# Optimization experiments

Measured on AMD Instinct MI355X. Metric: run time of the kernel, lower is better.

The kernel has to match this reference:

```python
import jax, jax.numpy as jnp
from jax import lax
import numpy as np

B, T, H, K = 128, 256, 768, 64


def setup_inputs() -> dict:
    key = jax.random.key(0)
    k1, k2, k3, k4 = jax.random.split(key, 4)
    hidden = jax.random.normal(k1, (B, T, H), dtype=jnp.float32)
    masks = jnp.ones((B, T), dtype=jnp.int32)
    target = jax.random.randint(k2, (B, T), 0, K, dtype=jnp.int32)
    W = jax.random.normal(k3, (H, K), dtype=jnp.float32) * 0.02
    b = jnp.zeros((K,), dtype=jnp.float32)
    transitions = jax.random.uniform(k4, (K, K), dtype=jnp.float32)
    return {"hidden": hidden, "masks": masks, "target": target,
            "W": W, "b": b, "transitions": transitions}


def _crf_log_norm(emissions, trans, seq_len):
    # emissions: [B,T,K]; forward algorithm (log-sum-exp recurrence over time)
    Tn = emissions.shape[1]
    alpha0 = emissions[:, 0]  # [B,K]

    def step(alpha, xs):
        emis_t, t = xs
        new = jax.nn.logsumexp(alpha[:, :, None] + trans[None], axis=1) + emis_t
        alpha = jnp.where((t < seq_len)[:, None], new, alpha)
        return alpha, None

    xs = (jnp.swapaxes(emissions[:, 1:], 0, 1), jnp.arange(1, Tn))
    alpha, _ = lax.scan(step, alpha0, xs)
    return jax.nn.logsumexp(alpha, axis=1)  # [B]


def _crf_sequence_score(emissions, tags, trans, seq_len):
    Tn = emissions.shape[1]
    t_idx = jnp.arange(Tn)
    valid = t_idx[None, :] < seq_len[:, None]  # [B,T]
    unary = jnp.take_along_axis(emissions, tags[..., None], axis=2)[..., 0]
    unary = jnp.sum(jnp.where(valid, unary, 0.0), axis=1)
    pair = trans[tags[:, :-1], tags[:, 1:]]  # [B,T-1]
    valid_pair = t_idx[1:][None, :] < seq_len[:, None]
    binary = jnp.sum(jnp.where(valid_pair, pair, 0.0), axis=1)
    return unary + binary


def _crf_decode(emissions, trans, seq_len):
    # Viterbi with backpointers; padded steps carry state (identity backptr)
    Bn, Tn, Kn = emissions.shape
    v0 = emissions[:, 0]

    def step(v, xs):
        emis_t, t = xs
        scores = v[:, :, None] + trans[None]  # [B, K_prev, K_cur]
        bp = jnp.argmax(scores, axis=1).astype(jnp.int32)
        new_v = jnp.max(scores, axis=1) + emis_t
        m = (t < seq_len)[:, None]
        v = jnp.where(m, new_v, v)
        bp = jnp.where(m, bp, jnp.arange(Kn, dtype=jnp.int32)[None])
        return v, bp

    xs = (jnp.swapaxes(emissions[:, 1:], 0, 1), jnp.arange(1, Tn))
    v, bps = lax.scan(step, v0, xs)  # bps: [T-1, B, K]
    best_score = jnp.max(v, axis=1)
    last_tag = jnp.argmax(v, axis=1).astype(jnp.int32)

    def back(tag, bp_t):
        prev = jnp.take_along_axis(bp_t, tag[:, None], axis=1)[:, 0]
        return prev, prev

    _, rev_tags = lax.scan(back, last_tag, bps, reverse=True)  # [T-1, B]
    path = jnp.concatenate([rev_tags, last_tag[None]], axis=0)  # [T, B]
    path = jnp.swapaxes(path, 0, 1)  # [B, T]
    valid = jnp.arange(Tn)[None, :] < seq_len[:, None]
    path = jnp.where(valid, path, 0)
    return path, best_score


def reference(hidden, masks, target, W, b, transitions):
    # dense projection (dropout omitted for determinism)
    emissions = jnp.einsum('bth,hk->btk', hidden, W) + b  # [B,T,K]
    seq_len = jnp.sum(masks, axis=1).astype(jnp.int32)
    log_norm = _crf_log_norm(emissions, transitions, seq_len)
    seq_score = _crf_sequence_score(emissions, target, transitions, seq_len)
    log_likelihood = seq_score - log_norm  # [B]
    decode_predict, _crf_scores = _crf_decode(emissions, transitions, seq_len)
    return decode_predict, log_likelihood
```

## Files before the change

kernel.cpp:

```cpp
#include <hip/hip_runtime.h>

#define B_ 128
#define T_ 256
#define H_ 768
#define K_ 64
#define BT_ (B_ * T_)

template <int CTRL>
__device__ __forceinline__ float dpp_mov_f(float x) {
    return __int_as_float(__builtin_amdgcn_update_dpp(
        __float_as_int(x), __float_as_int(x), CTRL, 0xF, 0xF, false));
}
__device__ __forceinline__ float wave_max64(float x) {
    x = fmaxf(x, dpp_mov_f<0x111>(x));
    x = fmaxf(x, dpp_mov_f<0x112>(x));
    x = fmaxf(x, dpp_mov_f<0x114>(x));
    x = fmaxf(x, dpp_mov_f<0x118>(x));
    x = fmaxf(x, dpp_mov_f<0x142>(x));
    x = fmaxf(x, dpp_mov_f<0x143>(x));
    return __int_as_float(__builtin_amdgcn_readlane(__float_as_int(x), 63));
}
__device__ __forceinline__ float readlane0_f(float x) {
    return __int_as_float(__builtin_amdgcn_readfirstlane(__float_as_int(x)));
}

__global__ __launch_bounds__(256, 2) void gemm_emis(const float* __restrict__ hidden,
                                                    const float* __restrict__ W,
                                                    const float* __restrict__ bias,
                                                    float* __restrict__ emis) {
    __shared__ __align__(16) float At[64 * 64];

    const int tid = threadIdx.x;
    const int lane = tid & 63;
    const int wv = tid >> 6;
    const int rowbase = blockIdx.x * 64;
    const int r0 = wv * 16;

    float acc[16];
    const float bb = bias[lane];
#pragma unroll
    for (int r = 0; r < 16; ++r) acc[r] = bb;

    for (int hb = 0; hb < H_; hb += 64) {
#pragma unroll
        for (int k = 0; k < 4; ++k) {
            int flat = tid + k * 256;
            int row = flat >> 4;
            int h4 = flat & 15;
            *(float4*)&At[row * 64 + h4 * 4] =
                *(const float4*)&hidden[(size_t)(rowbase + row) * H_ + hb + h4 * 4];
        }
        float Wr[64];
#pragma unroll
        for (int h = 0; h < 64; ++h) Wr[h] = W[(size_t)(hb + h) * K_ + lane];
        __syncthreads();

#pragma unroll
        for (int rg = 0; rg < 4; ++rg) {
#pragma unroll
            for (int h4 = 0; h4 < 16; ++h4) {
                float4 a0 = *(const float4*)&At[(r0 + rg * 4 + 0) * 64 + h4 * 4];
                float4 a1 = *(const float4*)&At[(r0 + rg * 4 + 1) * 64 + h4 * 4];
                float4 a2 = *(const float4*)&At[(r0 + rg * 4 + 2) * 64 + h4 * 4];
                float4 a3 = *(const float4*)&At[(r0 + rg * 4 + 3) * 64 + h4 * 4];
                float w0 = Wr[h4 * 4 + 0], w1 = Wr[h4 * 4 + 1];
                float w2 = Wr[h4 * 4 + 2], w3 = Wr[h4 * 4 + 3];
                acc[rg * 4 + 0] += a0.x * w0; acc[rg * 4 + 0] += a0.y * w1;
                acc[rg * 4 + 0] += a0.z * w2; acc[rg * 4 + 0] += a0.w * w3;
                acc[rg * 4 + 1] += a1.x * w0; acc[rg * 4 + 1] += a1.y * w1;
                acc[rg * 4 + 1] += a1.z * w2; acc[rg * 4 + 1] += a1.w * w3;
                acc[rg * 4 + 2] += a2.x * w0; acc[rg * 4 + 2] += a2.y * w1;
                acc[rg * 4 + 2] += a2.z * w2; acc[rg * 4 + 2] += a2.w * w3;
                acc[rg * 4 + 3] += a3.x * w0; acc[rg * 4 + 3] += a3.y * w1;
                acc[rg * 4 + 3] += a3.z * w2; acc[rg * 4 + 3] += a3.w * w3;
            }
        }
        __syncthreads();
    }
#pragma unroll
    for (int r = 0; r < 16; ++r)
        emis[(size_t)(rowbase + r0 + r) * K_ + lane] = acc[r];
}

__global__ __launch_bounds__(64, 1) void crf_kernel(const float* __restrict__ emis,
                                                    const int* __restrict__ masks,
                                                    const int* __restrict__ target,
                                                    const float* __restrict__ trans,
                                                    float* __restrict__ out) {
    __shared__ __align__(16) float vbuf[T_ * K_];
    __shared__ float tbuf[K_ * 65];

    const int lane = threadIdx.x;
    const int bid = blockIdx.x;
    const int b = (bid < B_) ? bid : bid - B_;

    int sl = 0;
#pragma unroll
    for (int k = 0; k < 4; ++k) sl += masks[b * T_ + lane + k * 64];
#pragma unroll
    for (int m = 32; m; m >>= 1) sl += __shfl_xor(sl, m, 64);
    const int seq_len = sl;

    const float* eb = emis + (size_t)b * (T_ * K_);

    if (bid < B_) {
        float Ecol[64];
#pragma unroll
        for (int i = 0; i < 64; ++i) Ecol[i] = __expf(trans[i * K_ + lane]);

        float e0 = eb[lane];
        float a00 = readlane0_f(e0);
        float r = __expf(e0 - a00);
        float c = a00;

        float e_cur = eb[K_ + lane];
        float e0_cur = readlane0_f(e_cur);
        float x_cur = __expf(e_cur - e0_cur);

        for (int t = 1; t < T_; ++t) {
            float e_nxt = (t < T_ - 1) ? eb[(t + 1) * K_ + lane] : 0.f;
            vbuf[lane] = r;
            float s0 = 0.f, s1 = 0.f, s2 = 0.f, s3 = 0.f;
#pragma unroll
            for (int i = 0; i < 16; ++i) {
                float4 p4 = *(const float4*)&vbuf[i * 4];
                s0 += p4.x * Ecol[i * 4 + 0];
                s1 += p4.y * Ecol[i * 4 + 1];
                s2 += p4.z * Ecol[i * 4 + 2];
                s3 += p4.w * Ecol[i * 4 + 3];
            }
            float S = (s0 + s1) + (s2 + s3);
            float S0 = readlane0_f(S);
            if (t < seq_len) {
                r = __fdividef(S * x_cur, S0);
                c += __logf(S0) + e0_cur;
            }
            e_cur = e_nxt;
            e0_cur = readlane0_f(e_cur);
            x_cur = __expf(e_cur - e0_cur);
        }
        float rs = r;
#pragma unroll
        for (int m = 32; m; m >>= 1) rs += __shfl_xor(rs, m, 64);
        float log_norm = c + __logf(rs);

        float sc = 0.f;
#pragma unroll
        for (int k = 0; k < 4; ++k) {
            int t = lane + k * 64;
            if (t < seq_len) {
                int tg = target[b * T_ + t];
                sc += eb[t * K_ + tg];
                if (t >= 1) sc += trans[target[b * T_ + t - 1] * K_ + tg];
            }
        }
#pragma unroll
        for (int m = 32; m; m >>= 1) sc += __shfl_xor(sc, m, 64);
        if (lane == 0) out[BT_ + b] = sc - log_norm;
    } else {
        float Tcol[64];
#pragma unroll
        for (int i = 0; i < 64; ++i) Tcol[i] = trans[i * K_ + lane];
        for (int idx = lane; idx < K_ * K_; idx += 64)
            tbuf[(idx >> 6) * 65 + (idx & 63)] = trans[idx];

        float v = eb[lane];
        vbuf[lane] = v;
        float e_cur = eb[K_ + lane];
        for (int t = 1; t < T_; ++t) {
            float e_nxt = (t < T_ - 1) ? eb[(t + 1) * K_ + lane] : 0.f;
            const float* vp = &vbuf[(t - 1) * K_];
            float mm[4];
            mm[0] = mm[1] = mm[2] = mm[3] = -3.4e38f;
#pragma unroll
            for (int i = 0; i < 16; ++i) {
                float4 v4 = *(const float4*)&vp[i * 4];
                float q = fmaxf(fmaxf(v4.x + Tcol[i * 4 + 0], v4.y + Tcol[i * 4 + 1]),
                                fmaxf(v4.z + Tcol[i * 4 + 2], v4.w + Tcol[i * 4 + 3]));
                mm[i & 3] = fmaxf(mm[i & 3], q);
            }
            float M = fmaxf(fmaxf(mm[0], mm[1]), fmaxf(mm[2], mm[3]));
            if (t < seq_len) v = M + e_cur;
            vbuf[t * K_ + lane] = v;
            e_cur = e_nxt;
        }

        float M = wave_max64(v);
        unsigned long long ball = __ballot(v >= M);
        int tag = (int)__builtin_ctzll(ball);

        int path[4];
#pragma unroll
        for (int k = 0; k < 4; ++k) path[k] = 0;
        if (lane == ((T_ - 1) & 63)) path[(T_ - 1) >> 6] = tag;

        float vpre = vbuf[(T_ - 2) * K_ + lane];
        for (int t = T_ - 1; t >= 1; --t) {
            float vnext = (t >= 2) ? vbuf[(t - 2) * K_ + lane] : 0.f;
            if (t < seq_len) {
                float s = vpre + tbuf[lane * 65 + tag];
                float Ms = wave_max64(s);
                unsigned long long bl = __ballot(s >= Ms);
                tag = (int)__builtin_ctzll(bl);
            }
            int p = t - 1;
            if (lane == (p & 63)) path[p >> 6] = tag;
            vpre = vnext;
        }
#pragma unroll
        for (int k = 0; k < 4; ++k) {
            int t = lane + k * 64;
            out[b * T_ + t] = (t < seq_len) ? (float)path[k] : 0.f;
        }
    }
}

extern "C" void kernel_launch(void* const* d_in, const int* in_sizes, int n_in,
                              void* d_out, int out_size, void* d_ws, size_t ws_size,
                              hipStream_t stream) {
    const float* hidden = (const float*)d_in[0];
    const int* masks    = (const int*)d_in[1];
    const int* target   = (const int*)d_in[2];
    const float* W      = (const float*)d_in[3];
    const float* bias   = (const float*)d_in[4];
    const float* trans  = (const float*)d_in[5];
    float* out = (float*)d_out;
    float* emis = (float*)d_ws;

    gemm_emis<<<dim3(BT_ / 64), dim3(256), 0, stream>>>(hidden, W, bias, emis);
    crf_kernel<<<dim3(2 * B_), dim3(64), 0, stream>>>(emis, masks, target, trans, out);
}
```

Before: 414.4 us.

## Restructure emission GEMM with transposed LDS tile, register prefetch, wave-uniform W loads

Rewrites the hidden×W projection kernel. It now uses 128-row blocks and stages a transposed 32-wide K slice of hidden in padded LDS. The next slice is prefetched into registers while the current one is computed. Each wave owns 16 output columns, and W is read with wave-uniform float4 loads that can become scalar/broadcast loads. Each lane computes 2 rows × 16 columns. The aim is to raise FMA-to-load ratio and hide global latency in the GEMM, which likely dominates alongside the serial CRF kernel. The costs are more register pressure and fewer blocks (256), which leaves roughly one block per CU.

```diff
diff --git a/kernel.cpp b/kernel.cpp
--- a/kernel.cpp
+++ b/kernel.cpp
@@ -24,62 +24,84 @@
     return __int_as_float(__builtin_amdgcn_readfirstlane(__float_as_int(x)));
 }
 
-__global__ __launch_bounds__(256, 2) void gemm_emis(const float* __restrict__ hidden,
-                                                    const float* __restrict__ W,
-                                                    const float* __restrict__ bias,
-                                                    float* __restrict__ emis) {
-    __shared__ __align__(16) float At[64 * 64];
+#define BK_ 32
+#define P_ 130
+__global__ __launch_bounds__(256) void gemm_emis(const float* __restrict__ hidden,
+                                                 const float* __restrict__ W,
+                                                 const float* __restrict__ bias,
+                                                 float* __restrict__ emis) {
+    __shared__ float At[BK_ * P_];
 
     const int tid = threadIdx.x;
     const int lane = tid & 63;
-    const int wv = tid >> 6;
-    const int rowbase = blockIdx.x * 64;
-    const int r0 = wv * 16;
-
-    float acc[16];
-    const float bb = bias[lane];
-#pragma unroll
-    for (int r = 0; r < 16; ++r) acc[r] = bb;
-
-    for (int hb = 0; hb < H_; hb += 64) {
-#pragma unroll
-        for (int k = 0; k < 4; ++k) {
-            int flat = tid + k * 256;
-            int row = flat >> 4;
-            int h4 = flat & 15;
-            *(float4*)&At[row * 64 + h4 * 4] =
-                *(const float4*)&hidden[(size_t)(rowbase + row) * H_ + hb + h4 * 4];
-        }
-        float Wr[64];
-#pragma unroll
-        for (int h = 0; h < 64; ++h) Wr[h] = W[(size_t)(hb + h) * K_ + lane];
+    const int wc = __builtin_amdgcn_readfirstlane((tid >> 6) * 16);
+    const int rowbase = blockIdx.x * 128;
+
+    const int srow = tid >> 3;
+    const int sh4 = tid & 7;
+
+    float acc0[16], acc1[16];
+#pragma unroll
+    for (int c = 0; c < 16; ++c) { acc0[c] = bias[wc + c]; acc1[c] = acc0[c]; }
+
+    float4 pf[4];
+#pragma unroll
+    for (int i = 0; i < 4; ++i)
+        pf[i] = *(const float4*)&hidden[(rowbase + srow + i * 32) * H_ + sh4 * 4];
+
+    for (int kb = 0; kb < H_ / BK_; ++kb) {
         __syncthreads();
-
-#pragma unroll
-        for (int rg = 0; rg < 4; ++rg) {
-#pragma unroll
-            for (int h4 = 0; h4 < 16; ++h4) {
-                float4 a0 = *(const float4*)&At[(r0 + rg * 4 + 0) * 64 + h4 * 4];
-                float4 a1 = *(const float4*)&At[(r0 + rg * 4 + 1) * 64 + h4 * 4];
-                float4 a2 = *(const float4*)&At[(r0 + rg * 4 + 2) * 64 + h4 * 4];
-                float4 a3 = *(const float4*)&At[(r0 + rg * 4 + 3) * 64 + h4 * 4];
-                float w0 = Wr[h4 * 4 + 0], w1 = Wr[h4 * 4 + 1];
-                float w2 = Wr[h4 * 4 + 2], w3 = Wr[h4 * 4 + 3];
-                acc[rg * 4 + 0] += a0.x * w0; acc[rg * 4 + 0] += a0.y * w1;
-                acc[rg * 4 + 0] += a0.z * w2; acc[rg * 4 + 0] += a0.w * w3;
-                acc[rg * 4 + 1] += a1.x * w0; acc[rg * 4 + 1] += a1.y * w1;
-                acc[rg * 4 + 1] += a1.z * w2; acc[rg * 4 + 1] += a1.w * w3;
-                acc[rg * 4 + 2] += a2.x * w0; acc[rg * 4 + 2] += a2.y * w1;
-                acc[rg * 4 + 2] += a2.z * w2; acc[rg * 4 + 2] += a2.w * w3;
-                acc[rg * 4 + 3] += a3.x * w0; acc[rg * 4 + 3] += a3.y * w1;
-                acc[rg * 4 + 3] += a3.z * w2; acc[rg * 4 + 3] += a3.w * w3;
-            }
+#pragma unroll
+        for (int i = 0; i < 4; ++i) {
+            int row = srow + i * 32;
+            At[(sh4 * 4 + 0) * P_ + row] = pf[i].x;
+            At[(sh4 * 4 + 1) * P_ + row] = pf[i].y;
+            At[(sh4 * 4 + 2) * P_ + row] = pf[i].z;
+            At[(sh4 * 4 + 3) * P_ + row] = pf[i].w;
         }
         __syncthreads();
+        if (kb + 1 < H_ / BK_) {
+#pragma unroll
+            for (int i = 0; i < 4; ++i)
+                pf[i] = *(const float4*)&hidden[(rowbase + srow + i * 32) * H_ +
+                                                (kb + 1) * BK_ + sh4 * 4];
+        }
+        const float* Wk = &W[(kb * BK_) * K_ + wc];
+#pragma unroll 8
+        for (int h = 0; h < BK_; ++h) {
+            float2 a = *(const float2*)&At[h * P_ + 2 * lane];
+            float4 w0 = *(const float4*)&Wk[h * K_ + 0];
+            float4 w1 = *(const float4*)&Wk[h * K_ + 4];
+            float4 w2 = *(const float4*)&Wk[h * K_ + 8];
+            float4 w3 = *(const float4*)&Wk[h * K_ + 12];
+            acc0[0]  += a.x * w0.x; acc1[0]  += a.y * w0.x;
+            acc0[1]  += a.x * w0.y; acc1[1]  += a.y * w0.y;
+            acc0[2]  += a.x * w0.z; acc1[2]  += a.y * w0.z;
+            acc0[3]  += a.x * w0.w; acc1[3]  += a.y * w0.w;
+            acc0[4]  += a.x * w1.x; acc1[4]  += a.y * w1.x;
+            acc0[5]  += a.x * w1.y; acc1[5]  += a.y * w1.y;
+            acc0[6]  += a.x * w1.z; acc1[6]  += a.y * w1.z;
+            acc0[7]  += a.x * w1.w; acc1[7]  += a.y * w1.w;
+            acc0[8]  += a.x * w2.x; acc1[8]  += a.y * w2.x;
+            acc0[9]  += a.x * w2.y; acc1[9]  += a.y * w2.y;
+            acc0[10] += a.x * w2.z; acc1[10] += a.y * w2.z;
+            acc0[11] += a.x * w2.w; acc1[11] += a.y * w2.w;
+            acc0[12] += a.x * w3.x; acc1[12] += a.y * w3.x;
+            acc0[13] += a.x * w3.y; acc1[13] += a.y * w3.y;
+            acc0[14] += a.x * w3.z; acc1[14] += a.y * w3.z;
+            acc0[15] += a.x * w3.w; acc1[15] += a.y * w3.w;
+        }
     }
-#pragma unroll
-    for (int r = 0; r < 16; ++r)
-        emis[(size_t)(rowbase + r0 + r) * K_ + lane] = acc[r];
+
+    float* e0 = &emis[(size_t)(rowbase + 2 * lane) * K_ + wc];
+    float* e1 = &emis[(size_t)(rowbase + 2 * lane + 1) * K_ + wc];
+#pragma unroll
+    for (int q = 0; q < 4; ++q) {
+        *(float4*)&e0[q * 4] = make_float4(acc0[q * 4], acc0[q * 4 + 1],
+                                           acc0[q * 4 + 2], acc0[q * 4 + 3]);
+        *(float4*)&e1[q * 4] = make_float4(acc1[q * 4], acc1[q * 4 + 1],
+                                           acc1[q * 4 + 2], acc1[q * 4 + 3]);
+    }
 }
 
 __global__ __launch_bounds__(64, 1) void crf_kernel(const float* __restrict__ emis,
@@ -227,6 +249,6 @@
     float* out = (float*)d_out;
     float* emis = (float*)d_ws;
 
-    gemm_emis<<<dim3(BT_ / 64), dim3(256), 0, stream>>>(hidden, W, bias, emis);
+    gemm_emis<<<dim3(BT_ / 128), dim3(256), 0, stream>>>(hidden, W, bias, emis);
     crf_kernel<<<dim3(2 * B_), dim3(64), 0, stream>>>(emis, masks, target, trans, out);
 }
```

After: 390.8 us. 1.06x faster.
